# Performance work log

Measured on AMD Instinct MI355X. Metric: run time of the kernel, lower is better.

## Reference

```python
import jax, jax.numpy as jnp
import numpy as np

B, L, D, H = 4, 2048, 1024, 16
HD = D // H

def setup_inputs() -> dict:
    key = jax.random.key(0)
    k1, k2, k3, k4 = jax.random.split(key, 4)
    return {
        "Q": jax.random.normal(k1, (B, L, D), dtype=jnp.float32),
        "K": jax.random.normal(k2, (B, L, D), dtype=jnp.float32),
        "V": jax.random.normal(k3, (B, L, D), dtype=jnp.float32),
        "W_out": jax.random.normal(k4, (D, D), dtype=jnp.float32) * (1.0 / np.sqrt(D)),
        "b_out": jnp.zeros((D,), dtype=jnp.float32),
    }

def reference(Q, K, V, W_out, b_out):
    b, l, d = Q.shape
    h, hd = H, d // H
    q = Q.reshape(b, l, h, hd)
    k = K.reshape(b, l, h, hd)
    v = V.reshape(b, l, h, hd)
    # energy: [b, h, q, k]
    energy = jnp.einsum('nqhd,nkhd->nhqk', q, k)
    # NOTE: original scales by sqrt(embed_dim), not sqrt(head_dim)
    attn = jax.nn.softmax(energy / jnp.sqrt(jnp.float32(d)), axis=-1)
    out = jnp.einsum('nhql,nlhd->nqhd', attn, v).reshape(b, l, d)
    # torch nn.Linear: x @ W.T + b
    return out @ W_out.T + b_out
```

## Files before the change

kernel.cpp:

```cpp
#include <hip/hip_runtime.h>
#include <hip/hip_bf16.h>


#define B_  4
#define L_  2048
#define D_  1024
#define H_  16

typedef float  f32x4  __attribute__((ext_vector_type(4)));
typedef short  bf16x8 __attribute__((ext_vector_type(8)));
typedef short  bf16x4 __attribute__((ext_vector_type(4)));

__device__ inline unsigned short f2bf(float x) {
    union { float f; unsigned u; } v; v.f = x;
    unsigned r = v.u + 0x7FFFu + ((v.u >> 16) & 1u);
    return (unsigned short)(r >> 16);
}
__device__ inline unsigned pack_trunc2(float lo, float hi) {
    union { float f; unsigned u; } a, b; a.f = lo; b.f = hi;
    return (a.u >> 16) | (b.u & 0xFFFF0000u);
}
__device__ inline float fast_exp2(float x) {
#if __has_builtin(__builtin_amdgcn_exp2f)
    return __builtin_amdgcn_exp2f(x);
#else
    return exp2f(x);
#endif
}
__device__ inline bf16x8 pack8s(float4 a, float4 b, float s) {
    bf16x8 r;
    r[0] = (short)f2bf(a.x * s); r[1] = (short)f2bf(a.y * s);
    r[2] = (short)f2bf(a.z * s); r[3] = (short)f2bf(a.w * s);
    r[4] = (short)f2bf(b.x * s); r[5] = (short)f2bf(b.y * s);
    r[6] = (short)f2bf(b.z * s); r[7] = (short)f2bf(b.w * s);
    return r;
}
__device__ inline void gld16(const void* g, void* l) {
    __builtin_amdgcn_global_load_lds(
        (const __attribute__((address_space(1))) void*)g,
        (__attribute__((address_space(3))) void*)l, 16, 0, 0);
}

__global__ __launch_bounds__(256) void convw_kernel(const float* __restrict__ W,
                                                    unsigned short* __restrict__ Wb) {
    int i = (blockIdx.x * 256 + threadIdx.x) * 4;
    float4 v = *(const float4*)&W[i];
    bf16x4 o;
    o[0] = (short)f2bf(v.x); o[1] = (short)f2bf(v.y);
    o[2] = (short)f2bf(v.z); o[3] = (short)f2bf(v.w);
    *(bf16x4*)&Wb[i] = o;
}

__global__ __launch_bounds__(256) void convk_kernel(const float* __restrict__ K,
                                                    unsigned short* __restrict__ Kb) {
    int o = blockIdx.x * 256 + threadIdx.x;
    int d8 = o & 7; int h = (o >> 3) & 15; int key = (o >> 7) & 2047; int b = o >> 18;
    size_t base = ((size_t)(b * L_ + key) * H_ + h) * 64;
    const float* p = K + base + d8 * 8;
    float4 a = *(const float4*)p, c = *(const float4*)(p + 4);
    bf16x8 r;
    r[0] = (short)f2bf(a.x); r[1] = (short)f2bf(a.y); r[2] = (short)f2bf(a.z); r[3] = (short)f2bf(a.w);
    r[4] = (short)f2bf(c.x); r[5] = (short)f2bf(c.y); r[6] = (short)f2bf(c.z); r[7] = (short)f2bf(c.w);
    *(bf16x8*)&Kb[base + ((d8 * 8) ^ ((key & 7) * 8))] = r;
}

__global__ __launch_bounds__(256) void convv_kernel(const float* __restrict__ V,
                                                    unsigned short* __restrict__ Vb) {
    __shared__ __align__(16) unsigned short T[64 * 72];
    int tid = threadIdx.x;
    int kb_ = blockIdx.x & 31, bh = blockIdx.x >> 5;
    int b = bh >> 4, h = bh & 15, k0 = kb_ * 64;
    int kl = tid >> 4;
    int d4 = (tid & 15) * 4;
    #pragma unroll
    for (int pp = 0; pp < 4; ++pp) {
        int key = pp * 16 + kl;
        const float* p = V + ((size_t)(b * L_ + k0 + key)) * D_ + h * 64 + d4;
        float4 v = *(const float4*)p;
        T[(d4 + 0) * 72 + key] = f2bf(v.x);
        T[(d4 + 1) * 72 + key] = f2bf(v.y);
        T[(d4 + 2) * 72 + key] = f2bf(v.z);
        T[(d4 + 3) * 72 + key] = f2bf(v.w);
    }
    __syncthreads();
    #pragma unroll
    for (int i = 0; i < 2; ++i) {
        int c = i * 256 + tid; int d = c >> 3, ch = c & 7;
        bf16x8 v = *(const bf16x8*)&T[d * 72 + ch * 8];
        *(bf16x8*)&Vb[((size_t)(b * H_ + h) * 64 + d) * L_ + k0 + ((ch ^ (d & 7)) * 8)] = v;
    }
}

__global__ __launch_bounds__(256, 4) void attn_kernel(const float* __restrict__ Qg,
                                                      const unsigned short* __restrict__ Kb,
                                                      const unsigned short* __restrict__ Vb,
                                                      unsigned short* __restrict__ Og) {
    __shared__ unsigned short Ks[2][64 * 64];
    __shared__ unsigned short Vt[2][64 * 64];

    const int tid  = threadIdx.x;
    const int w    = tid >> 6;
    const int lane = tid & 63;
    const int l16  = lane & 15;
    const int quad = lane >> 4;

    const int x   = blockIdx.x;
    const int idx = x >> 3;
    const int bh  = (x & 7) * 8 + (idx & 7);
    const int qb  = idx >> 3;
    const int bz  = bh >> 4;
    const int h   = bh & 15;
    const int q0  = qb * 128;

    const float qscale = 0.04508422f;
    bf16x8 aq[2][2];
    #pragma unroll
    for (int qt = 0; qt < 2; ++qt) {
        const int qrow = q0 + w * 32 + qt * 16 + l16;
        const float* qp = Qg + ((size_t)(bz * L_ + qrow)) * D_ + h * 64 + quad * 8;
        aq[qt][0] = pack8s(*(const float4*)qp,        *(const float4*)(qp + 4),  qscale);
        aq[qt][1] = pack8s(*(const float4*)(qp + 32), *(const float4*)(qp + 36), qscale);
    }

    f32x4 o[2][4];
    float lsum[2] = {0.f, 0.f};
    #pragma unroll
    for (int qt = 0; qt < 2; ++qt)
        #pragma unroll
        for (int i = 0; i < 4; ++i) o[qt][i] = (f32x4){0.f, 0.f, 0.f, 0.f};

    const unsigned short* Kbh = Kb + ((size_t)bz * L_ * H_ + h) * 64;
    const unsigned short* Vbh = Vb + (size_t)(bz * H_ + h) * 64 * L_;
    const int sw = (l16 & 7) * 8;
    const int hi = quad >> 1;
    const int i0 = (quad & 1) * 32 + l16;
    const int i1 = i0 + 16;

    #define ISSUE(T, BUF)                                                           \
        {                                                                           \
            int k0_ = (T) * 64;                                                     \
            _Pragma("unroll")                                                       \
            for (int i = 0; i < 2; ++i) {                                           \
                int c = i * 256 + tid; int rr = c >> 3, jj = c & 7;                 \
                gld16(Kbh + (size_t)(k0_ + rr) * (H_ * 64) + jj * 8,                \
                      (char*)Ks[BUF] + (i * 256 + w * 64) * 16);                    \
                gld16(Vbh + (size_t)rr * L_ + k0_ + jj * 8,                         \
                      (char*)Vt[BUF] + (i * 256 + w * 64) * 16);                    \
            }                                                                       \
        }

    ISSUE(0, 0)

    for (int t = 0; t < 32; ++t) {
        __syncthreads();
        if (t < 31) ISSUE(t + 1, (t + 1) & 1)
        const unsigned short* ks = Ks[t & 1];
        const unsigned short* vt = Vt[t & 1];

        f32x4 s[2][4];
        #pragma unroll
        for (int nt = 0; nt < 4; ++nt) {
            bf16x8 k0f = *(const bf16x8*)&ks[(nt * 16 + l16) * 64 + ((quad * 8) ^ sw)];
            bf16x8 k1f = *(const bf16x8*)&ks[(nt * 16 + l16) * 64 + ((32 + quad * 8) ^ sw)];
            #pragma unroll
            for (int qt = 0; qt < 2; ++qt) {
                f32x4 z = (f32x4){0.f, 0.f, 0.f, 0.f};
                z = __builtin_amdgcn_mfma_f32_16x16x32_bf16(k0f, aq[qt][0], z, 0, 0, 0);
                s[qt][nt] = __builtin_amdgcn_mfma_f32_16x16x32_bf16(k1f, aq[qt][1], z, 0, 0, 0);
            }
        }

        unsigned packed[2][4][2];
        #pragma unroll
        for (int qt = 0; qt < 2; ++qt)
            #pragma unroll
            for (int nt = 0; nt < 4; ++nt) {
                float p0 = fast_exp2(s[qt][nt][0]), p1 = fast_exp2(s[qt][nt][1]);
                float p2 = fast_exp2(s[qt][nt][2]), p3 = fast_exp2(s[qt][nt][3]);
                lsum[qt] += (p0 + p1) + (p2 + p3);
                packed[qt][nt][0] = pack_trunc2(p0, p1);
                packed[qt][nt][1] = pack_trunc2(p2, p3);
            }

        bf16x8 pav[2][2];
        #pragma unroll
        for (int qt = 0; qt < 2; ++qt) {
            union { int i[4]; bf16x8 v; } u0, u1;
            #pragma unroll
            for (int fp = 0; fp < 4; ++fp) {
                int src = (fp & 2) ? i1 : i0;
                int f   = fp & 1;
                int lo0 = __shfl((int)packed[qt][0][f], src);
                int hi0 = __shfl((int)packed[qt][1][f], src);
                u0.i[fp] = hi ? hi0 : lo0;
                int lo1 = __shfl((int)packed[qt][2][f], src);
                int hi1 = __shfl((int)packed[qt][3][f], src);
                u1.i[fp] = hi ? hi1 : lo1;
            }
            pav[qt][0] = u0.v; pav[qt][1] = u1.v;
        }

        #pragma unroll
        for (int dt = 0; dt < 4; ++dt) {
            bf16x8 v0 = *(const bf16x8*)&vt[(dt * 16 + l16) * 64 + ((quad * 8)      ^ sw)];
            bf16x8 v1 = *(const bf16x8*)&vt[(dt * 16 + l16) * 64 + ((32 + quad * 8) ^ sw)];
            #pragma unroll
            for (int qt = 0; qt < 2; ++qt) {
                o[qt][dt] = __builtin_amdgcn_mfma_f32_16x16x32_bf16(pav[qt][0], v0, o[qt][dt], 0, 0, 0);
                o[qt][dt] = __builtin_amdgcn_mfma_f32_16x16x32_bf16(pav[qt][1], v1, o[qt][dt], 0, 0, 0);
            }
        }
    }

    float tot[2];
    #pragma unroll
    for (int qt = 0; qt < 2; ++qt) {
        float v = lsum[qt];
        v += __shfl_xor(v, 16); v += __shfl_xor(v, 32);
        tot[qt] = v;
    }
    #pragma unroll
    for (int qt = 0; qt < 2; ++qt)
        #pragma unroll
        for (int r = 0; r < 4; ++r) {
            float tv  = __shfl(tot[qt], quad * 4 + r);
            float inv = 1.0f / tv;
            int q = q0 + w * 32 + qt * 16 + quad * 4 + r;
            size_t rowb = ((size_t)(bz * L_ + q)) * D_ + h * 64;
            #pragma unroll
            for (int dt = 0; dt < 4; ++dt)
                Og[rowb + dt * 16 + l16] = f2bf(o[qt][dt][r] * inv);
        }
}

__global__ __launch_bounds__(256, 2) void proj_kernel(const unsigned short* __restrict__ Og,
                                                      const unsigned short* __restrict__ Wb,
                                                      const float* __restrict__ bias,
                                                      float* __restrict__ Yg) {
    __shared__ unsigned short As[2][128 * 64];
    __shared__ unsigned short Bs[2][128 * 64];

    const int tid  = threadIdx.x;
    const int w    = tid >> 6;
    const int lane = tid & 63;
    const int l16  = lane & 15;
    const int quad = lane >> 4;
    const int wm   = w & 1, wn = w >> 1;

    const int m0 = blockIdx.x * 128;
    const int n0 = blockIdx.y * 128;

    f32x4 acc[4][4];
    #pragma unroll
    for (int i = 0; i < 4; ++i)
        #pragma unroll
        for (int j = 0; j < 4; ++j) acc[i][j] = (f32x4){0.f, 0.f, 0.f, 0.f};

    #define PISSUE(T, BUF)                                                          \
        {                                                                           \
            int kt_ = (T) * 64;                                                     \
            _Pragma("unroll")                                                       \
            for (int i = 0; i < 4; ++i) {                                           \
                int c = i * 256 + tid; int row = c >> 3, p = c & 7;                 \
                int j = p ^ (row & 7);                                              \
                gld16(&Og[(size_t)(m0 + row) * 1024 + kt_ + j * 8],                 \
                      (char*)As[BUF] + (i * 256 + w * 64) * 16);                    \
                gld16(&Wb[(size_t)(n0 + row) * 1024 + kt_ + j * 8],                 \
                      (char*)Bs[BUF] + (i * 256 + w * 64) * 16);                    \
            }                                                                       \
        }

    PISSUE(0, 0)

    for (int t = 0; t < 16; ++t) {
        __syncthreads();
        if (t < 15) PISSUE(t + 1, (t + 1) & 1)
        const unsigned short* as = As[t & 1];
        const unsigned short* bs = Bs[t & 1];

        #pragma unroll
        for (int ksq = 0; ksq < 2; ++ksq) {
            bf16x8 a[4], b[4];
            #pragma unroll
            for (int mt = 0; mt < 4; ++mt) {
                int row = wm * 64 + mt * 16 + l16;
                a[mt] = *(const bf16x8*)&as[row * 64 + (((ksq * 4 + quad) ^ (l16 & 7)) * 8)];
            }
            #pragma unroll
            for (int nt = 0; nt < 4; ++nt) {
                int row = wn * 64 + nt * 16 + l16;
                b[nt] = *(const bf16x8*)&bs[row * 64 + (((ksq * 4 + quad) ^ (l16 & 7)) * 8)];
            }
            #pragma unroll
            for (int mt = 0; mt < 4; ++mt)
                #pragma unroll
                for (int nt = 0; nt < 4; ++nt)
                    acc[mt][nt] = __builtin_amdgcn_mfma_f32_16x16x32_bf16(a[mt], b[nt], acc[mt][nt], 0, 0, 0);
        }
    }

    #pragma unroll
    for (int mt = 0; mt < 4; ++mt)
        #pragma unroll
        for (int nt = 0; nt < 4; ++nt) {
            int e = n0 + wn * 64 + nt * 16 + l16;
            float bv = bias[e];
            #pragma unroll
            for (int r = 0; r < 4; ++r) {
                int m = m0 + wm * 64 + mt * 16 + quad * 4 + r;
                Yg[(size_t)m * 1024 + e] = acc[mt][nt][r] + bv;
            }
        }
}

extern "C" void kernel_launch(void* const* d_in, const int* in_sizes, int n_in,
                              void* d_out, int out_size, void* d_ws, size_t ws_size,
                              hipStream_t stream) {
    const float* Q    = (const float*)d_in[0];
    const float* K    = (const float*)d_in[1];
    const float* V    = (const float*)d_in[2];
    const float* W    = (const float*)d_in[3];
    const float* bias = (const float*)d_in[4];
    float* Y = (float*)d_out;

    unsigned short* Og = (unsigned short*)d_ws;
    unsigned short* Wb = (unsigned short*)((char*)d_ws + (size_t)16 * 1024 * 1024);
    unsigned short* Kb = (unsigned short*)d_out;
    unsigned short* Vb = Kb + (size_t)B_ * H_ * L_ * 64;

    convw_kernel<<<D_ * D_ / (256 * 4), 256, 0, stream>>>(W, Wb);
    convk_kernel<<<B_ * L_ * H_ * 8 / 256, 256, 0, stream>>>(K, Kb);
    convv_kernel<<<B_ * H_ * (L_ / 64), 256, 0, stream>>>(V, Vb);
    attn_kernel<<<B_ * H_ * (L_ / 128), 256, 0, stream>>>(Q, Kb, Vb, Og);
    dim3 pg(B_ * L_ / 128, D_ / 128);
    proj_kernel<<<pg, 256, 0, stream>>>(Og, Wb, bias, Y);
}
```

Baseline: 260.5 us.

## Store LDS tiles in MFMA fragment order instead of XOR-swizzled rows

The global-to-LDS loads in the attention and projection kernels now place data so that each wave's MFMA operand fragment is one contiguous 8-lane-stride block. This lets LDS reads index simply by lane, without XOR swizzle arithmetic, while avoiding bank conflicts. Because the swizzle is gone, the dedicated K conversion kernel is replaced by the plain elementwise convert kernel, and V no longer needs swizzled stores. The new global load pattern gathers 16-row stripes, which may reduce coalescing per wave.

```diff
diff --git a/kernel.cpp b/kernel.cpp
--- a/kernel.cpp
+++ b/kernel.cpp
@@ -51,19 +51,6 @@
     *(bf16x4*)&Wb[i] = o;
 }
 
-__global__ __launch_bounds__(256) void convk_kernel(const float* __restrict__ K,
-                                                    unsigned short* __restrict__ Kb) {
-    int o = blockIdx.x * 256 + threadIdx.x;
-    int d8 = o & 7; int h = (o >> 3) & 15; int key = (o >> 7) & 2047; int b = o >> 18;
-    size_t base = ((size_t)(b * L_ + key) * H_ + h) * 64;
-    const float* p = K + base + d8 * 8;
-    float4 a = *(const float4*)p, c = *(const float4*)(p + 4);
-    bf16x8 r;
-    r[0] = (short)f2bf(a.x); r[1] = (short)f2bf(a.y); r[2] = (short)f2bf(a.z); r[3] = (short)f2bf(a.w);
-    r[4] = (short)f2bf(c.x); r[5] = (short)f2bf(c.y); r[6] = (short)f2bf(c.z); r[7] = (short)f2bf(c.w);
-    *(bf16x8*)&Kb[base + ((d8 * 8) ^ ((key & 7) * 8))] = r;
-}
-
 __global__ __launch_bounds__(256) void convv_kernel(const float* __restrict__ V,
                                                     unsigned short* __restrict__ Vb) {
     __shared__ __align__(16) unsigned short T[64 * 72];
@@ -87,7 +74,7 @@
     for (int i = 0; i < 2; ++i) {
         int c = i * 256 + tid; int d = c >> 3, ch = c & 7;
         bf16x8 v = *(const bf16x8*)&T[d * 72 + ch * 8];
-        *(bf16x8*)&Vb[((size_t)(b * H_ + h) * 64 + d) * L_ + k0 + ((ch ^ (d & 7)) * 8)] = v;
+        *(bf16x8*)&Vb[((size_t)(b * H_ + h) * 64 + d) * L_ + k0 + ch * 8] = v;
     }
 }
 
@@ -131,7 +118,6 @@
 
     const unsigned short* Kbh = Kb + ((size_t)bz * L_ * H_ + h) * 64;
     const unsigned short* Vbh = Vb + (size_t)(bz * H_ + h) * 64 * L_;
-    const int sw = (l16 & 7) * 8;
     const int hi = quad >> 1;
     const int i0 = (quad & 1) * 32 + l16;
     const int i1 = i0 + 16;
@@ -141,10 +127,13 @@
             int k0_ = (T) * 64;                                                     \
             _Pragma("unroll")                                                       \
             for (int i = 0; i < 2; ++i) {                                           \
-                int c = i * 256 + tid; int rr = c >> 3, jj = c & 7;                 \
-                gld16(Kbh + (size_t)(k0_ + rr) * (H_ * 64) + jj * 8,                \
+                int c   = i * 256 + tid;                                            \
+                int tt  = (c >> 7) & 3;                       \
+                int jj  = ((c >> 6) & 1) * 4 + ((c >> 4) & 3);           \
+                int e16 = c & 15;                                                   \
+                gld16(Kbh + (size_t)(k0_ + tt * 16 + e16) * (H_ * 64) + jj * 8,     \
                       (char*)Ks[BUF] + (i * 256 + w * 64) * 16);                    \
-                gld16(Vbh + (size_t)rr * L_ + k0_ + jj * 8,                         \
+                gld16(Vbh + (size_t)(tt * 16 + e16) * L_ + k0_ + jj * 8,            \
                       (char*)Vt[BUF] + (i * 256 + w * 64) * 16);                    \
             }                                                                       \
         }
@@ -160,8 +149,8 @@
         f32x4 s[2][4];
         #pragma unroll
         for (int nt = 0; nt < 4; ++nt) {
-            bf16x8 k0f = *(const bf16x8*)&ks[(nt * 16 + l16) * 64 + ((quad * 8) ^ sw)];
-            bf16x8 k1f = *(const bf16x8*)&ks[(nt * 16 + l16) * 64 + ((32 + quad * 8) ^ sw)];
+            bf16x8 k0f = *(const bf16x8*)&ks[(nt * 128 + lane) * 8];
+            bf16x8 k1f = *(const bf16x8*)&ks[(nt * 128 + 64 + lane) * 8];
             #pragma unroll
             for (int qt = 0; qt < 2; ++qt) {
                 f32x4 z = (f32x4){0.f, 0.f, 0.f, 0.f};
@@ -202,8 +191,8 @@
 
         #pragma unroll
         for (int dt = 0; dt < 4; ++dt) {
-            bf16x8 v0 = *(const bf16x8*)&vt[(dt * 16 + l16) * 64 + ((quad * 8)      ^ sw)];
-            bf16x8 v1 = *(const bf16x8*)&vt[(dt * 16 + l16) * 64 + ((32 + quad * 8) ^ sw)];
+            bf16x8 v0 = *(const bf16x8*)&vt[(dt * 128 + lane) * 8];
+            bf16x8 v1 = *(const bf16x8*)&vt[(dt * 128 + 64 + lane) * 8];
             #pragma unroll
             for (int qt = 0; qt < 2; ++qt) {
                 o[qt][dt] = __builtin_amdgcn_mfma_f32_16x16x32_bf16(pav[qt][0], v0, o[qt][dt], 0, 0, 0);
@@ -261,11 +250,14 @@
             int kt_ = (T) * 64;                                                     \
             _Pragma("unroll")                                                       \
             for (int i = 0; i < 4; ++i) {                                           \
-                int c = i * 256 + tid; int row = c >> 3, p = c & 7;                 \
-                int j = p ^ (row & 7);                                              \
-                gld16(&Og[(size_t)(m0 + row) * 1024 + kt_ + j * 8],                 \
+                int c   = i * 256 + tid;                                            \
+                int hm  = c >> 9;                               \
+                int mt  = (c >> 7) & 3;                                             \
+                int jj  = ((c >> 6) & 1) * 4 + ((c >> 4) & 3);                      \
+                int row = hm * 64 + mt * 16 + (c & 15);                             \
+                gld16(&Og[(size_t)(m0 + row) * 1024 + kt_ + jj * 8],                \
                       (char*)As[BUF] + (i * 256 + w * 64) * 16);                    \
-                gld16(&Wb[(size_t)(n0 + row) * 1024 + kt_ + j * 8],                 \
+                gld16(&Wb[(size_t)(n0 + row) * 1024 + kt_ + jj * 8],                \
                       (char*)Bs[BUF] + (i * 256 + w * 64) * 16);                    \
             }                                                                       \
         }
@@ -282,15 +274,11 @@
         for (int ksq = 0; ksq < 2; ++ksq) {
             bf16x8 a[4], b[4];
             #pragma unroll
-            for (int mt = 0; mt < 4; ++mt) {
-                int row = wm * 64 + mt * 16 + l16;
-                a[mt] = *(const bf16x8*)&as[row * 64 + (((ksq * 4 + quad) ^ (l16 & 7)) * 8)];
-            }
-            #pragma unroll
-            for (int nt = 0; nt < 4; ++nt) {
-                int row = wn * 64 + nt * 16 + l16;
-                b[nt] = *(const bf16x8*)&bs[row * 64 + (((ksq * 4 + quad) ^ (l16 & 7)) * 8)];
-            }
+            for (int mt = 0; mt < 4; ++mt)
+                a[mt] = *(const bf16x8*)&as[(((wm * 4 + mt) * 2 + ksq) * 64 + lane) * 8];
+            #pragma unroll
+            for (int nt = 0; nt < 4; ++nt)
+                b[nt] = *(const bf16x8*)&bs[(((wn * 4 + nt) * 2 + ksq) * 64 + lane) * 8];
             #pragma unroll
             for (int mt = 0; mt < 4; ++mt)
                 #pragma unroll
@@ -329,7 +317,7 @@
     unsigned short* Vb = Kb + (size_t)B_ * H_ * L_ * 64;
 
     convw_kernel<<<D_ * D_ / (256 * 4), 256, 0, stream>>>(W, Wb);
-    convk_kernel<<<B_ * L_ * H_ * 8 / 256, 256, 0, stream>>>(K, Kb);
+    convw_kernel<<<B_ * L_ * D_ / (256 * 4), 256, 0, stream>>>(K, Kb);
     convv_kernel<<<B_ * H_ * (L_ / 64), 256, 0, stream>>>(V, Vb);
     attn_kernel<<<B_ * H_ * (L_ / 128), 256, 0, stream>>>(Q, Kb, Vb, Og);
     dim3 pg(B_ * L_ / 128, D_ / 128);
```

After: 278.9 us. 7.1% more time.
